# Performance work log

Hardware: AMD Instinct MI355X
Metric: run time of the kernel (lower is better)

Reference implementation:

```python
import jax, jax.numpy as jnp
import numpy as np

NEG_SLOPE = 0.2
N_NODES = 50000
N_EDGES = 800000
NUM_GRAPHS = 128
IN_F, HID_F, OUT_F = 64, 64, 64


def _gat_layer(x, src, dst, W, a_src, a_dst, b, n_nodes):
    # x: [N, Fin] -> out: [N, Fout]; single-head PyG GATConv with self-loops
    xp = x @ W                                   # [N, Fout]
    alpha_src = xp @ a_src                       # [N]
    alpha_dst = xp @ a_dst                       # [N]
    e = jax.nn.leaky_relu(alpha_src[src] + alpha_dst[dst], NEG_SLOPE)  # [E]
    # segment softmax over incoming edges of each dst node
    m = jax.ops.segment_max(e, dst, num_segments=n_nodes)
    ex = jnp.exp(e - m[dst])
    denom = jax.ops.segment_sum(ex, dst, num_segments=n_nodes)
    alpha = ex / denom[dst]                      # [E]
    out = jax.ops.segment_sum(alpha[:, None] * xp[src], dst, num_segments=n_nodes)
    return out + b


def setup_inputs() -> dict:
    key = jax.random.key(0)
    ks = jax.random.split(key, 12)
    x = jax.random.normal(ks[0], (N_NODES, IN_F), dtype=jnp.float32)
    edge_index = jax.random.randint(ks[1], (2, N_EDGES), 0, N_NODES, dtype=jnp.int64 if jax.config.jax_enable_x64 else jnp.int32)
    batch = jnp.sort(jax.random.randint(ks[2], (N_NODES,), 0, NUM_GRAPHS, dtype=edge_index.dtype))
    s = 0.1
    W1 = jax.random.normal(ks[3], (IN_F, HID_F), dtype=jnp.float32) * s
    att_src1 = jax.random.normal(ks[4], (HID_F,), dtype=jnp.float32) * s
    att_dst1 = jax.random.normal(ks[5], (HID_F,), dtype=jnp.float32) * s
    b1 = jax.random.normal(ks[6], (HID_F,), dtype=jnp.float32) * s
    W2 = jax.random.normal(ks[7], (HID_F, OUT_F), dtype=jnp.float32) * s
    att_src2 = jax.random.normal(ks[8], (OUT_F,), dtype=jnp.float32) * s
    att_dst2 = jax.random.normal(ks[9], (OUT_F,), dtype=jnp.float32) * s
    b2 = jax.random.normal(ks[10], (OUT_F,), dtype=jnp.float32) * s
    return {"x": x, "edge_index": edge_index, "batch": batch,
            "W1": W1, "att_src1": att_src1, "att_dst1": att_dst1, "b1": b1,
            "W2": W2, "att_src2": att_src2, "att_dst2": att_dst2, "b2": b2}


def reference(x, edge_index, batch, W1, att_src1, att_dst1, b1, W2, att_src2, att_dst2, b2):
    n = x.shape[0]
    # add self-loops (PyG GATConv default)
    loops = jnp.arange(n, dtype=edge_index.dtype)
    src = jnp.concatenate([edge_index[0], loops])
    dst = jnp.concatenate([edge_index[1], loops])
    h = _gat_layer(x, src, dst, W1, att_src1, att_dst1, b1, n)
    h = jax.nn.relu(h)  # dropout = identity at eval
    h = _gat_layer(h, src, dst, W2, att_src2, att_dst2, b2, n)
    h = jax.nn.relu(h)
    # scatter_mean over graphs
    sums = jax.ops.segment_sum(h, batch, num_segments=NUM_GRAPHS)
    counts = jax.ops.segment_sum(jnp.ones((n,), dtype=h.dtype), batch, num_segments=NUM_GRAPHS)
    return sums / jnp.maximum(counts, 1.0)[:, None]
```

## Files before the change

### kernel.cpp

```cpp
#include <hip/hip_runtime.h>
#include <hip/hip_fp16.h>

#define FEAT 64
#define BK   64
#define CAP  1536
#define MAXB 1024
#define SEPT 16
#define CHUNK (256 * SEPT)
#define LG   4

typedef _Float16 f16;
typedef __attribute__((ext_vector_type(8))) _Float16 f16x8;
typedef __attribute__((ext_vector_type(4))) float    f32x4;

struct GemmSm {
    union {
        struct { f16 Xs[64][72]; f16 Wt[64][72]; };
        float Cs[4][16][68];
    };
    float asl[64], adl[64];
};

__device__ __forceinline__ void gemm_tile(
    GemmSm& sm, int row0, const float* __restrict__ xin,
    const float* __restrict__ W, const float* __restrict__ avs,
    const float* __restrict__ avd, unsigned* __restrict__ xph,
    float* __restrict__ as_, float* __restrict__ ad_, int n)
{
    const int t = threadIdx.x;
    const int lane = t & 63;
    const int wave = t >> 6;

    if (t < 64) sm.asl[t] = avs[t];
    else if (t < 128) sm.adl[t - 64] = avd[t - 64];

    for (int i = t; i < 64 * 16; i += 256) {
        const int r = i >> 4, c4 = (i & 15) << 2;
        const int gr = row0 + r;
        float4 v = make_float4(0.f, 0.f, 0.f, 0.f);
        if (gr < n) v = *(const float4*)(xin + (size_t)gr * FEAT + c4);
        sm.Xs[r][c4 + 0] = (f16)v.x; sm.Xs[r][c4 + 1] = (f16)v.y;
        sm.Xs[r][c4 + 2] = (f16)v.z; sm.Xs[r][c4 + 3] = (f16)v.w;
    }
    for (int i = t; i < 64 * 16; i += 256) {
        const int k = i >> 4, c4 = (i & 15) << 2;
        const float4 v = *(const float4*)(W + k * FEAT + c4);
        sm.Wt[c4 + 0][k] = (f16)v.x; sm.Wt[c4 + 1][k] = (f16)v.y;
        sm.Wt[c4 + 2][k] = (f16)v.z; sm.Wt[c4 + 3][k] = (f16)v.w;
    }
    __syncthreads();

    const int mrow = (wave << 4) + (lane & 15);
    const int kg = lane >> 4;
    const f16x8 a0 = *(const f16x8*)(&sm.Xs[mrow][kg * 8]);
    const f16x8 a1 = *(const f16x8*)(&sm.Xs[mrow][32 + kg * 8]);

    f32x4 acc[4];
#pragma unroll
    for (int nt = 0; nt < 4; ++nt) {
        const int ncol = nt * 16 + (lane & 15);
        const f16x8 b0 = *(const f16x8*)(&sm.Wt[ncol][kg * 8]);
        const f16x8 b1 = *(const f16x8*)(&sm.Wt[ncol][32 + kg * 8]);
        f32x4 c = {0.f, 0.f, 0.f, 0.f};
        c = __builtin_amdgcn_mfma_f32_16x16x32_f16(a0, b0, c, 0, 0, 0);
        c = __builtin_amdgcn_mfma_f32_16x16x32_f16(a1, b1, c, 0, 0, 0);
        acc[nt] = c;
    }
    __syncthreads();

#pragma unroll
    for (int nt = 0; nt < 4; ++nt)
#pragma unroll
        for (int reg = 0; reg < 4; ++reg)
            sm.Cs[wave][(lane >> 4) * 4 + reg][nt * 16 + (lane & 15)] = acc[nt][reg];

    for (int i = lane; i < 16 * 32; i += 64) {
        const int r = i >> 5, fp = i & 31;
        const int node = row0 + (wave << 4) + r;
        if (node < n) {
            const __half2 pk = __floats2half2_rn(sm.Cs[wave][r][2 * fp],
                                                 sm.Cs[wave][r][2 * fp + 1]);
            xph[(size_t)node * 32 + fp] = *(const unsigned*)&pk;
        }
    }
    {
        const int r = lane >> 2, q = lane & 3;
        float s1 = 0.f, s2 = 0.f;
#pragma unroll
        for (int j = 0; j < 16; ++j) {
            const int c = q * 16 + j;
            const float v = sm.Cs[wave][r][c];
            s1 += v * sm.asl[c];
            s2 += v * sm.adl[c];
        }
        s1 += __shfl_xor(s1, 1); s1 += __shfl_xor(s1, 2);
        s2 += __shfl_xor(s2, 1); s2 += __shfl_xor(s2, 2);
        const int node = row0 + (wave << 4) + r;
        if (q == 0 && node < n) { as_[node] = s1; ad_[node] = s2; }
    }
}

__global__ __launch_bounds__(256) void scatter_gemm1_kernel(
    const int* __restrict__ src, const int* __restrict__ dst,
    int* __restrict__ bcur, unsigned* __restrict__ ebuf,
    const float* __restrict__ x, const float* __restrict__ W,
    const float* __restrict__ a_src, const float* __restrict__ a_dst,
    unsigned* __restrict__ xph, float* __restrict__ as_, float* __restrict__ ad_,
    int n, int E, int nbuck, int nchunks)
{
    __shared__ union {
        struct {
            unsigned staged[CHUNK];
            int hist[MAXB]; int lofs[MAXB]; int base[MAXB];
        } s;
        GemmSm g;
    } sm;

    const int t = threadIdx.x;
    const int lane = t & 63;
    const int wave = t >> 6;

    if (blockIdx.x < (unsigned)nchunks) {
        for (int i = t; i < nbuck; i += 256) sm.s.hist[i] = 0;
        __syncthreads();

        const int e0 = blockIdx.x * CHUNK;
        const int total = min(E - e0, CHUNK);

        unsigned code[SEPT]; int bk[SEPT], rk[SEPT];
#pragma unroll
        for (int k = 0; k < SEPT; ++k) {
            const int e = e0 + t + k * 256;
            bk[k] = -1;
            if (e < E) {
                const int s_ = src[e], d = dst[e];
                bk[k] = d >> 6;
                code[k] = ((unsigned)s_ << 6) | (unsigned)(d & 63);
                rk[k] = atomicAdd(&sm.s.hist[bk[k]], 1);
            }
        }
        __syncthreads();

        if (wave == 0) {
            int carry = 0;
            for (int b0 = 0; b0 < nbuck; b0 += 64) {
                const int idx = b0 + lane;
                int v = (idx < nbuck) ? sm.s.hist[idx] : 0;
                const int orig = v;
#pragma unroll
                for (int o = 1; o < 64; o <<= 1) {
                    const int u = __shfl_up(v, o);
                    if (lane >= o) v += u;
                }
                if (idx < nbuck) sm.s.lofs[idx] = v - orig + carry;
                carry += __shfl(v, 63);
            }
        }
        __syncthreads();
        for (int i = t; i < nbuck; i += 256) {
            const int hv = sm.s.hist[i];
            sm.s.base[i] = hv ? atomicAdd(&bcur[i], hv) : 0;
        }
        __syncthreads();

#pragma unroll
        for (int k = 0; k < SEPT; ++k) {
            if (bk[k] >= 0)
                sm.s.staged[sm.s.lofs[bk[k]] + rk[k]] =
                    ((unsigned)bk[k] << 22) | code[k];
        }
        __syncthreads();

        for (int i = t; i < total; i += 256) {
            const unsigned e = sm.s.staged[i];
            const int bkt = e >> 22;
            const int pos = sm.s.base[bkt] + (i - sm.s.lofs[bkt]);
            if (pos < CAP) ebuf[(size_t)bkt * CAP + pos] = e & 0x3FFFFFu;
        }
    } else {
        gemm_tile(sm.g, (blockIdx.x - nchunks) * 64, x, W, a_src, a_dst,
                  xph, as_, ad_, n);
    }
}

struct PC {
    int node, g, gc, st, en;
    float w0, w1, w2, w3, asg;
    uint4 x0, x1, x2, x3, xg;
};

__device__ __forceinline__ void fma8(float* a, const uint4 xv, const float wv)
{
    const __half2 p0 = *(const __half2*)&xv.x;
    const __half2 p1 = *(const __half2*)&xv.y;
    const __half2 p2 = *(const __half2*)&xv.z;
    const __half2 p3 = *(const __half2*)&xv.w;
    a[0] += wv * __low2float(p0);  a[1] += wv * __high2float(p0);
    a[2] += wv * __low2float(p1);  a[3] += wv * __high2float(p1);
    a[4] += wv * __low2float(p2);  a[5] += wv * __high2float(p2);
    a[6] += wv * __low2float(p3);  a[7] += wv * __high2float(p3);
}

__device__ __forceinline__ void pc_issue(PC& P, int pair, int np, int q, int fo,
    int g0, int n, const int* startsL, const unsigned* scode, const float* sw,
    const float* __restrict__ as_, const uint4* __restrict__ xph4)
{
    P.node = pair * 2 + np;
    P.g  = g0 + P.node;
    P.gc = (P.g < n) ? P.g : (n - 1);
    P.st = startsL[P.node];
    P.en = startsL[P.node + 1];
    const int i0 = P.st + q;
    unsigned c0 = 0, c1 = 0, c2 = 0, c3 = 0;
    P.w0 = 0.f; P.w1 = 0.f; P.w2 = 0.f; P.w3 = 0.f;
    if (i0      < P.en) { c0 = scode[i0];      P.w0 = sw[i0]; }
    if (i0 + 4  < P.en) { c1 = scode[i0 + 4];  P.w1 = sw[i0 + 4]; }
    if (i0 + 8  < P.en) { c2 = scode[i0 + 8];  P.w2 = sw[i0 + 8]; }
    if (i0 + 12 < P.en) { c3 = scode[i0 + 12]; P.w3 = sw[i0 + 12]; }
    P.x0 = xph4[(size_t)(c0 >> 6) * 8 + fo];
    P.x1 = xph4[(size_t)(c1 >> 6) * 8 + fo];
    P.x2 = xph4[(size_t)(c2 >> 6) * 8 + fo];
    P.x3 = xph4[(size_t)(c3 >> 6) * 8 + fo];
    P.xg = xph4[(size_t)P.gc * 8 + fo];
    P.asg = as_[P.gc];
}

__device__ __forceinline__ void pc_consume(const PC& P, int q, int fo,
    const unsigned* scode, const float* sw, const uint4* __restrict__ xph4,
    float* a, float& wsum)
{
    fma8(a, P.x0, P.w0); fma8(a, P.x1, P.w1);
    fma8(a, P.x2, P.w2); fma8(a, P.x3, P.w3);
    wsum += (P.w0 + P.w1) + (P.w2 + P.w3);

    int i = P.st + q + 16;
    for (; i + 12 < P.en; i += 16) {
        const unsigned c0 = scode[i];
        const unsigned c1 = scode[i + 4];
        const unsigned c2 = scode[i + 8];
        const unsigned c3 = scode[i + 12];
        const float w0 = sw[i], w1 = sw[i + 4], w2 = sw[i + 8], w3 = sw[i + 12];
        const uint4 x0 = xph4[(size_t)(c0 >> 6) * 8 + fo];
        const uint4 x1 = xph4[(size_t)(c1 >> 6) * 8 + fo];
        const uint4 x2 = xph4[(size_t)(c2 >> 6) * 8 + fo];
        const uint4 x3 = xph4[(size_t)(c3 >> 6) * 8 + fo];
        fma8(a, x0, w0); fma8(a, x1, w1); fma8(a, x2, w2); fma8(a, x3, w3);
        wsum += (w0 + w1) + (w2 + w3);
    }
    for (; i < P.en; i += 4) {
        const unsigned c0 = scode[i];
        const float w0 = sw[i];
        const uint4 xv = xph4[(size_t)(c0 >> 6) * 8 + fo];
        fma8(a, xv, w0);
        wsum += w0;
    }
}

__device__ __forceinline__ void pc_reduce(float* a, float& wsum)
{
#pragma unroll
    for (int j = 0; j < 8; ++j) {
        a[j] += __shfl_xor(a[j], 8);
        a[j] += __shfl_xor(a[j], 16);
    }
    wsum += __shfl_xor(wsum, 8);
    wsum += __shfl_xor(wsum, 16);
}

__device__ __forceinline__ void pc_epi_h(const PC& P, int q, int fo,
    const float* adb, float* a, float wsum, const float4 bA, const float4 bB,
    float* __restrict__ hout, int hstride, int n)
{
    pc_reduce(a, wsum);
    float tt = P.asg + adb[P.node];
    tt = (tt >= 0.f) ? tt : 0.2f * tt;
    const float wself = __expf(tt);
    const __half2 s0 = *(const __half2*)&P.xg.x;
    const __half2 s1 = *(const __half2*)&P.xg.y;
    const __half2 s2 = *(const __half2*)&P.xg.z;
    const __half2 s3 = *(const __half2*)&P.xg.w;
    const float dinv = 1.f / (wsum + wself);

    if (q == 0 && P.g < n) {
        float4 vA, vB;
        vA.x = fmaxf((a[0] + wself * __low2float(s0))  * dinv + bA.x, 0.f);
        vA.y = fmaxf((a[1] + wself * __high2float(s0)) * dinv + bA.y, 0.f);
        vA.z = fmaxf((a[2] + wself * __low2float(s1))  * dinv + bA.z, 0.f);
        vA.w = fmaxf((a[3] + wself * __high2float(s1)) * dinv + bA.w, 0.f);
        vB.x = fmaxf((a[4] + wself * __low2float(s2))  * dinv + bB.x, 0.f);
        vB.y = fmaxf((a[5] + wself * __high2float(s2)) * dinv + bB.y, 0.f);
        vB.z = fmaxf((a[6] + wself * __low2float(s3))  * dinv + bB.z, 0.f);
        vB.w = fmaxf((a[7] + wself * __high2float(s3)) * dinv + bB.w, 0.f);
        *(float4*)(hout + (size_t)P.node * hstride + 8 * fo)     = vA;
        *(float4*)(hout + (size_t)P.node * hstride + 8 * fo + 4) = vB;
    }
}

__device__ __forceinline__ void pc_epi_pool(const PC& P, int q, int fo,
    int wave, int np, const float* adb, float* a, float wsum,
    const float4 bA, const float4 bB, const int* batchL, int gbase,
    float (*gpartW)[2][LG][FEAT], float* __restrict__ osum, int n)
{
    pc_reduce(a, wsum);
    float tt = P.asg + adb[P.node];
    tt = (tt >= 0.f) ? tt : 0.2f * tt;
    const float wself = __expf(tt);
    const __half2 s0 = *(const __half2*)&P.xg.x;
    const __half2 s1 = *(const __half2*)&P.xg.y;
    const __half2 s2 = *(const __half2*)&P.xg.z;
    const __half2 s3 = *(const __half2*)&P.xg.w;
    const float dinv = 1.f / (wsum + wself);

    if (q == 0 && P.g < n) {
        float4 vA, vB;
        vA.x = fmaxf((a[0] + wself * __low2float(s0))  * dinv + bA.x, 0.f);
        vA.y = fmaxf((a[1] + wself * __high2float(s0)) * dinv + bA.y, 0.f);
        vA.z = fmaxf((a[2] + wself * __low2float(s1))  * dinv + bA.z, 0.f);
        vA.w = fmaxf((a[3] + wself * __high2float(s1)) * dinv + bA.w, 0.f);
        vB.x = fmaxf((a[4] + wself * __low2float(s2))  * dinv + bB.x, 0.f);
        vB.y = fmaxf((a[5] + wself * __high2float(s2)) * dinv + bB.y, 0.f);
        vB.z = fmaxf((a[6] + wself * __low2float(s3))  * dinv + bB.z, 0.f);
        vB.w = fmaxf((a[7] + wself * __high2float(s3)) * dinv + bB.w, 0.f);

        const int lg = batchL[P.node] - gbase;
        if (lg < LG) {
            float* p = &gpartW[wave][np][lg][8 * fo];
            float4 oA = *(float4*)p;
            float4 oB = *(float4*)(p + 4);
            oA.x += vA.x; oA.y += vA.y; oA.z += vA.z; oA.w += vA.w;
            oB.x += vB.x; oB.y += vB.y; oB.z += vB.z; oB.w += vB.w;
            *(float4*)p = oA;
            *(float4*)(p + 4) = oB;
        } else {
            float* o = osum + (size_t)batchL[P.node] * FEAT + 8 * fo;
            atomicAdd(o + 0, vA.x); atomicAdd(o + 1, vA.y);
            atomicAdd(o + 2, vA.z); atomicAdd(o + 3, vA.w);
            atomicAdd(o + 4, vB.x); atomicAdd(o + 5, vB.y);
            atomicAdd(o + 6, vB.z); atomicAdd(o + 7, vB.w);
        }
    }
}

__global__ __launch_bounds__(512) void sortagg1_gemm2_kernel(
    const int* __restrict__ bcur, unsigned* __restrict__ ebuf,
    int* __restrict__ startsG,
    const float* __restrict__ asA, const float* __restrict__ adA,
    const uint4* __restrict__ xphA, const float* __restrict__ b1,
    const float* __restrict__ W2, const float* __restrict__ asrc2,
    const float* __restrict__ adst2,
    unsigned* __restrict__ xphB, float* __restrict__ asB, float* __restrict__ adB,
    int n)
{
    __shared__ float htile[64][68];
    __shared__ union {
        struct { unsigned scode[CAP]; float sw[CAP]; int hist[BK]; int cur[BK]; } a;
        GemmSm g;
    } sm;
    __shared__ int starts[BK + 1];
    __shared__ float adb[BK];

    const int b = blockIdx.x;
    const int t = threadIdx.x;
    const int lane = t & 63, wave = t >> 6;
    const int g0 = b * BK;
    const int row0 = g0;

    if (t < BK) {
        sm.a.hist[t] = 0;
        adb[t] = (g0 + t < n) ? adA[g0 + t] : 0.f;
    }
    __syncthreads();

    int cnt = bcur[b];
    if (cnt > CAP) cnt = CAP;
    unsigned* eb = ebuf + (size_t)b * CAP;

    unsigned c[3];
#pragma unroll
    for (int k = 0; k < 3; ++k) {
        const int i = t + k * 512;
        if (i < cnt) { c[k] = eb[i]; atomicAdd(&sm.a.hist[c[k] & 63], 1); }
    }
    __syncthreads();
    if (wave == 0) {
        int v = sm.a.hist[lane];
#pragma unroll
        for (int o = 1; o < 64; o <<= 1) {
            const int u = __shfl_up(v, o);
            if (lane >= o) v += u;
        }
        starts[lane + 1] = v;
        sm.a.cur[lane] = v - sm.a.hist[lane];
        if (lane == 0) starts[0] = 0;
    }
    __syncthreads();
#pragma unroll
    for (int k = 0; k < 3; ++k) {
        const int i = t + k * 512;
        if (i < cnt) { const int p = atomicAdd(&sm.a.cur[c[k] & 63], 1); sm.a.scode[p] = c[k]; }
    }
    __syncthreads();

    unsigned cc[3]; float vv[3];
#pragma unroll
    for (int k = 0; k < 3; ++k) {
        const int i = t + k * 512;
        if (i < cnt) { cc[k] = sm.a.scode[i]; eb[i] = cc[k]; vv[k] = asA[cc[k] >> 6]; }
    }
    if (t <= BK) startsG[b * (BK + 1) + t] = starts[t];
#pragma unroll
    for (int k = 0; k < 3; ++k) {
        const int i = t + k * 512;
        if (i < cnt) {
            float tt = vv[k] + adb[cc[k] & 63];
            tt = (tt >= 0.f) ? tt : 0.2f * tt;
            sm.a.sw[i] = __expf(tt);
        }
    }
    __syncthreads();

    {
        const int np = lane >> 5;
        const int q  = (lane >> 3) & 3;
        const int fo = lane & 7;
        const float4 bA = *(const float4*)(b1 + 8 * fo);
        const float4 bB = *(const float4*)(b1 + 8 * fo + 4);
#pragma unroll
        for (int gsel = 0; gsel < 2; ++gsel) {
            PC A, B;
            pc_issue(A, wave + 8 * gsel,      np, q, fo, g0, n,
                     starts, sm.a.scode, sm.a.sw, asA, xphA);
            pc_issue(B, wave + 8 * gsel + 16, np, q, fo, g0, n,
                     starts, sm.a.scode, sm.a.sw, asA, xphA);
            float aA[8] = {0.f, 0.f, 0.f, 0.f, 0.f, 0.f, 0.f, 0.f};
            float wsA = 0.f;
            pc_consume(A, q, fo, sm.a.scode, sm.a.sw, xphA, aA, wsA);
            pc_epi_h(A, q, fo, adb, aA, wsA, bA, bB, &htile[0][0], 68, n);
            float aB[8] = {0.f, 0.f, 0.f, 0.f, 0.f, 0.f, 0.f, 0.f};
            float wsB = 0.f;
            pc_consume(B, q, fo, sm.a.scode, sm.a.sw, xphA, aB, wsB);
            pc_epi_h(B, q, fo, adb, aB, wsB, bA, bB, &htile[0][0], 68, n);
        }
    }
    __syncthreads();

    if (t < 64) sm.g.asl[t] = asrc2[t];
    else if (t < 128) sm.g.adl[t - 64] = adst2[t - 64];

    for (int i = t; i < 64 * 16; i += 512) {
        const int r = i >> 4, c4 = (i & 15) << 2;
        const float4 v = *(const float4*)(&htile[r][c4]);
        sm.g.Xs[r][c4 + 0] = (f16)v.x; sm.g.Xs[r][c4 + 1] = (f16)v.y;
        sm.g.Xs[r][c4 + 2] = (f16)v.z; sm.g.Xs[r][c4 + 3] = (f16)v.w;
    }
    for (int i = t; i < 64 * 16; i += 512) {
        const int k = i >> 4, c4 = (i & 15) << 2;
        const float4 v = *(const float4*)(W2 + k * FEAT + c4);
        sm.g.Wt[c4 + 0][k] = (f16)v.x; sm.g.Wt[c4 + 1][k] = (f16)v.y;
        sm.g.Wt[c4 + 2][k] = (f16)v.z; sm.g.Wt[c4 + 3][k] = (f16)v.w;
    }
    __syncthreads();

    f32x4 acc[4];
    if (wave < 4) {
        const int mrow = (wave << 4) + (lane & 15);
        const int kg = lane >> 4;
        const f16x8 a0 = *(const f16x8*)(&sm.g.Xs[mrow][kg * 8]);
        const f16x8 a1 = *(const f16x8*)(&sm.g.Xs[mrow][32 + kg * 8]);
#pragma unroll
        for (int nt = 0; nt < 4; ++nt) {
            const int ncol = nt * 16 + (lane & 15);
            const f16x8 b0 = *(const f16x8*)(&sm.g.Wt[ncol][kg * 8]);
            const f16x8 b1v = *(const f16x8*)(&sm.g.Wt[ncol][32 + kg * 8]);
            f32x4 cacc = {0.f, 0.f, 0.f, 0.f};
            cacc = __builtin_amdgcn_mfma_f32_16x16x32_f16(a0, b0, cacc, 0, 0, 0);
            cacc = __builtin_amdgcn_mfma_f32_16x16x32_f16(a1, b1v, cacc, 0, 0, 0);
            acc[nt] = cacc;
        }
    }
    __syncthreads();
    if (wave < 4) {
#pragma unroll
        for (int nt = 0; nt < 4; ++nt)
#pragma unroll
            for (int reg = 0; reg < 4; ++reg)
                sm.g.Cs[wave][(lane >> 4) * 4 + reg][nt * 16 + (lane & 15)] = acc[nt][reg];
    }
    __syncthreads();

    for (int i = t; i < 64 * 32; i += 512) {
        const int r = i >> 5, fp = i & 31;
        const int node = row0 + r;
        if (node < n) {
            const __half2 pk = __floats2half2_rn(sm.g.Cs[r >> 4][r & 15][2 * fp],
                                                 sm.g.Cs[r >> 4][r & 15][2 * fp + 1]);
            xphB[(size_t)node * 32 + fp] = *(const unsigned*)&pk;
        }
    }
    if (t < 256) {
        const int r = t >> 2, q = t & 3;
        float s1 = 0.f, s2 = 0.f;
#pragma unroll
        for (int j = 0; j < 16; ++j) {
            const int cidx = q * 16 + j;
            const float v = sm.g.Cs[r >> 4][r & 15][cidx];
            s1 += v * sm.g.asl[cidx];
            s2 += v * sm.g.adl[cidx];
        }
        s1 += __shfl_xor(s1, 1); s1 += __shfl_xor(s1, 2);
        s2 += __shfl_xor(s2, 1); s2 += __shfl_xor(s2, 2);
        const int node = row0 + r;
        if (q == 0 && node < n) { asB[node] = s1; adB[node] = s2; }
    }
}

__global__ __launch_bounds__(512) void agg2_pool_kernel(
    const unsigned* __restrict__ ebuf, const int* __restrict__ startsG,
    const float* __restrict__ as_, const float* __restrict__ ad_,
    const uint4* __restrict__ xph4, const float* __restrict__ bias,
    const int* __restrict__ batch, float* __restrict__ gpart,
    float* __restrict__ osum, int n)
{
    __shared__ unsigned scode[CAP];
    __shared__ float    sw[CAP];
    __shared__ int startsL[BK + 1];
    __shared__ float adb[BK];
    __shared__ int batchL[BK];
    __shared__ float gpartW[8][2][LG][FEAT];

    const int b = blockIdx.x;
    const int t = threadIdx.x;
    const int lane = t & 63, wave = t >> 6;
    const int g0 = b * BK;

    if (t < BK) {
        const int g = g0 + t;
        adb[t] = (g < n) ? ad_[g] : 0.f;
        batchL[t] = batch[(g < n) ? g : (n - 1)];
    }
    if (t <= BK) startsL[t] = startsG[b * (BK + 1) + t];
    for (int i = t; i < 8 * 2 * LG * FEAT; i += 512) ((float*)gpartW)[i] = 0.f;
    __syncthreads();

    const int cnt = startsL[BK];
    const unsigned* eb = ebuf + (size_t)b * CAP;

    unsigned cc[3]; float vv[3];
#pragma unroll
    for (int k = 0; k < 3; ++k) {
        const int i = t + k * 512;
        if (i < cnt) { cc[k] = eb[i]; vv[k] = as_[cc[k] >> 6]; }
    }
#pragma unroll
    for (int k = 0; k < 3; ++k) {
        const int i = t + k * 512;
        if (i < cnt) {
            float tt = vv[k] + adb[cc[k] & 63];
            tt = (tt >= 0.f) ? tt : 0.2f * tt;
            scode[i] = cc[k]; sw[i] = __expf(tt);
        }
    }
    __syncthreads();

    {
        const int np = lane >> 5;
        const int q  = (lane >> 3) & 3;
        const int fo = lane & 7;
        const int gbase = batchL[0];
        const float4 bA = *(const float4*)(bias + 8 * fo);
        const float4 bB = *(const float4*)(bias + 8 * fo + 4);
#pragma unroll
        for (int gsel = 0; gsel < 2; ++gsel) {
            PC A, B;
            pc_issue(A, wave + 8 * gsel,      np, q, fo, g0, n,
                     startsL, scode, sw, as_, xph4);
            pc_issue(B, wave + 8 * gsel + 16, np, q, fo, g0, n,
                     startsL, scode, sw, as_, xph4);
            float aA[8] = {0.f, 0.f, 0.f, 0.f, 0.f, 0.f, 0.f, 0.f};
            float wsA = 0.f;
            pc_consume(A, q, fo, scode, sw, xph4, aA, wsA);
            pc_epi_pool(A, q, fo, wave, np, adb, aA, wsA, bA, bB,
                        batchL, gbase, gpartW, osum, n);
            float aB[8] = {0.f, 0.f, 0.f, 0.f, 0.f, 0.f, 0.f, 0.f};
            float wsB = 0.f;
            pc_consume(B, q, fo, scode, sw, xph4, aB, wsB);
            pc_epi_pool(B, q, fo, wave, np, adb, aB, wsB, bA, bB,
                        batchL, gbase, gpartW, osum, n);
        }
    }
    __syncthreads();

    if (t < LG * FEAT) {
        const int lg = t >> 6, f = t & 63;
        float s = 0.f;
#pragma unroll
        for (int w = 0; w < 8; ++w)
            s += gpartW[w][0][lg][f] + gpartW[w][1][lg][f];
        gpart[((size_t)b * LG + lg) * FEAT + f] = s;
    }
}

__device__ __forceinline__ int lower_bound_i(const int* a, int n, int key)
{
    int lo = 0, hi = n;
    while (lo < hi) {
        const int mid = (lo + hi) >> 1;
        if (a[mid] < key) lo = mid + 1; else hi = mid;
    }
    return lo;
}

__global__ __launch_bounds__(64) void pool_reduce_kernel(
    const float* __restrict__ gpart, const float* __restrict__ osum,
    const int* __restrict__ batch, float* __restrict__ out, int n, int G)
{
    const int g = blockIdx.x;
    const int lane = threadIdx.x;

    const int lo = lower_bound_i(batch, n, g);
    const int hi = lower_bound_i(batch, n, g + 1);

    float s = osum[(size_t)g * FEAT + lane];
    if (lo < hi) {
        const int b0 = lo >> 6, b1 = (hi - 1) >> 6;
        for (int b = b0; b <= b1; ++b) {
            const int base = batch[b << 6];
            const int lg = g - base;
            if (lg >= 0 && lg < LG)
                s += gpart[((size_t)b * LG + lg) * FEAT + lane];
        }
    }
    out[(size_t)g * FEAT + lane] = s / fmaxf((float)(hi - lo), 1.f);
}

extern "C" void kernel_launch(void* const* d_in, const int* in_sizes, int n_in,
                              void* d_out, int out_size, void* d_ws, size_t ws_size,
                              hipStream_t stream)
{
    const float* x      = (const float*)d_in[0];
    const int*   ei     = (const int*)d_in[1];
    const int*   batch  = (const int*)d_in[2];
    const float* W1     = (const float*)d_in[3];
    const float* asrc1  = (const float*)d_in[4];
    const float* adst1  = (const float*)d_in[5];
    const float* b1     = (const float*)d_in[6];
    const float* W2     = (const float*)d_in[7];
    const float* asrc2  = (const float*)d_in[8];
    const float* adst2  = (const float*)d_in[9];
    const float* b2     = (const float*)d_in[10];

    const int N = in_sizes[2];
    const int E = in_sizes[1] / 2;
    const int G = out_size / FEAT;

    const int* src = ei;
    const int* dst = ei + E;

    const int nbuck   = (N + BK - 1) / BK;
    const int nchunks = (E + CHUNK - 1) / CHUNK;
    const int gemmBlocks = (N + 63) / 64;

    unsigned* xphA    = (unsigned*)d_ws;
    unsigned* xphB    = xphA + (size_t)N * 32;
    float*    asA     = (float*)(xphB + (size_t)N * 32);
    float*    adA     = asA + N;
    float*    asB     = adA + N;
    float*    adB     = asB + N;
    int*      bcur    = (int*)(adB + N);
    float*    osum    = (float*)(bcur + nbuck);
    unsigned* ebuf    = (unsigned*)(osum + (size_t)G * FEAT);
    int*      startsG = (int*)(ebuf + (size_t)nbuck * CAP);
    float*    gpart   = (float*)(startsG + nbuck * (BK + 1));

    hipMemsetAsync(bcur, 0,
                   (size_t)nbuck * sizeof(int) + (size_t)G * FEAT * sizeof(float),
                   stream);
    scatter_gemm1_kernel<<<nchunks + gemmBlocks, 256, 0, stream>>>(
        src, dst, bcur, ebuf, x, W1, asrc1, adst1, xphA, asA, adA,
        N, E, nbuck, nchunks);
    sortagg1_gemm2_kernel<<<nbuck, 512, 0, stream>>>(
        bcur, ebuf, startsG, asA, adA, (const uint4*)xphA, b1,
        W2, asrc2, adst2, xphB, asB, adB, N);
    agg2_pool_kernel<<<nbuck, 512, 0, stream>>>(
        ebuf, startsG, asB, adB, (const uint4*)xphB, b2,
        batch, gpart, osum, N);
    pool_reduce_kernel<<<G, 64, 0, stream>>>(gpart, osum, batch,
                                             (float*)d_out, N, G);
}
```

Baseline: 171.6 us.

## Remap aggregation to one node per wave with 8 edges in flight

The aggregation mapping changes from two nodes per wave (8 feature lanes × 4 edge lanes, uint4 loads) to one node per wave (16 feature lanes × 4 edge lanes, uint2 loads), with 8 gathers issued up front per lane. This gives more memory-level parallelism per node and drops the 16-wide unrolled loop. Layer-1 output is written straight into an fp16 shared tile that feeds the MFMA GEMM, removing the fp32 htile and its conversion pass. Pool partials are now added to osum with atomics inside agg2, so the final kernel only normalises, at the cost of extra global atomics and launch-bounds occupancy hints.

Result: slower. 179.5 us (+4.6%).

```diff
diff --git a/kernel.cpp b/kernel.cpp
--- a/kernel.cpp
+++ b/kernel.cpp
@@ -183,175 +183,143 @@
     }
 }
 
-struct PC {
+struct PC2 {
     int node, g, gc, st, en;
-    float w0, w1, w2, w3, asg;
-    uint4 x0, x1, x2, x3, xg;
+    float w[8], asg;
+    uint2 xs[8], xg;
 };
 
-__device__ __forceinline__ void fma8(float* a, const uint4 xv, const float wv)
+__device__ __forceinline__ void fma4(float* a, const uint2 xv, const float wv)
 {
     const __half2 p0 = *(const __half2*)&xv.x;
     const __half2 p1 = *(const __half2*)&xv.y;
-    const __half2 p2 = *(const __half2*)&xv.z;
-    const __half2 p3 = *(const __half2*)&xv.w;
-    a[0] += wv * __low2float(p0);  a[1] += wv * __high2float(p0);
-    a[2] += wv * __low2float(p1);  a[3] += wv * __high2float(p1);
-    a[4] += wv * __low2float(p2);  a[5] += wv * __high2float(p2);
-    a[6] += wv * __low2float(p3);  a[7] += wv * __high2float(p3);
-}
-
-__device__ __forceinline__ void pc_issue(PC& P, int pair, int np, int q, int fo,
+    a[0] += wv * __low2float(p0); a[1] += wv * __high2float(p0);
+    a[2] += wv * __low2float(p1); a[3] += wv * __high2float(p1);
+}
+
+__device__ __forceinline__ void pc2_issue(PC2& P, int node, int q, int fo,
     int g0, int n, const int* startsL, const unsigned* scode, const float* sw,
-    const float* __restrict__ as_, const uint4* __restrict__ xph4)
-{
-    P.node = pair * 2 + np;
-    P.g  = g0 + P.node;
+    const float* __restrict__ as_, const uint2* __restrict__ xph2)
+{
+    P.node = node;
+    P.g  = g0 + node;
     P.gc = (P.g < n) ? P.g : (n - 1);
-    P.st = startsL[P.node];
-    P.en = startsL[P.node + 1];
+    P.st = startsL[node];
+    P.en = startsL[node + 1];
     const int i0 = P.st + q;
-    unsigned c0 = 0, c1 = 0, c2 = 0, c3 = 0;
-    P.w0 = 0.f; P.w1 = 0.f; P.w2 = 0.f; P.w3 = 0.f;
-    if (i0      < P.en) { c0 = scode[i0];      P.w0 = sw[i0]; }
-    if (i0 + 4  < P.en) { c1 = scode[i0 + 4];  P.w1 = sw[i0 + 4]; }
-    if (i0 + 8  < P.en) { c2 = scode[i0 + 8];  P.w2 = sw[i0 + 8]; }
-    if (i0 + 12 < P.en) { c3 = scode[i0 + 12]; P.w3 = sw[i0 + 12]; }
-    P.x0 = xph4[(size_t)(c0 >> 6) * 8 + fo];
-    P.x1 = xph4[(size_t)(c1 >> 6) * 8 + fo];
-    P.x2 = xph4[(size_t)(c2 >> 6) * 8 + fo];
-    P.x3 = xph4[(size_t)(c3 >> 6) * 8 + fo];
-    P.xg = xph4[(size_t)P.gc * 8 + fo];
+    unsigned c[8];
+#pragma unroll
+    for (int j = 0; j < 8; ++j) {
+        const int i = i0 + 4 * j;
+        c[j] = 0u; P.w[j] = 0.f;
+        if (i < P.en) { c[j] = scode[i]; P.w[j] = sw[i]; }
+    }
+#pragma unroll
+    for (int j = 0; j < 8; ++j)
+        P.xs[j] = xph2[(size_t)(c[j] >> 6) * 16 + fo];
+    P.xg = xph2[(size_t)P.gc * 16 + fo];
     P.asg = as_[P.gc];
 }
 
-__device__ __forceinline__ void pc_consume(const PC& P, int q, int fo,
-    const unsigned* scode, const float* sw, const uint4* __restrict__ xph4,
+__device__ __forceinline__ void pc2_consume(const PC2& P, int q, int fo,
+    const unsigned* scode, const float* sw, const uint2* __restrict__ xph2,
     float* a, float& wsum)
 {
-    fma8(a, P.x0, P.w0); fma8(a, P.x1, P.w1);
-    fma8(a, P.x2, P.w2); fma8(a, P.x3, P.w3);
-    wsum += (P.w0 + P.w1) + (P.w2 + P.w3);
-
-    int i = P.st + q + 16;
-    for (; i + 12 < P.en; i += 16) {
-        const unsigned c0 = scode[i];
-        const unsigned c1 = scode[i + 4];
-        const unsigned c2 = scode[i + 8];
-        const unsigned c3 = scode[i + 12];
-        const float w0 = sw[i], w1 = sw[i + 4], w2 = sw[i + 8], w3 = sw[i + 12];
-        const uint4 x0 = xph4[(size_t)(c0 >> 6) * 8 + fo];
-        const uint4 x1 = xph4[(size_t)(c1 >> 6) * 8 + fo];
-        const uint4 x2 = xph4[(size_t)(c2 >> 6) * 8 + fo];
-        const uint4 x3 = xph4[(size_t)(c3 >> 6) * 8 + fo];
-        fma8(a, x0, w0); fma8(a, x1, w1); fma8(a, x2, w2); fma8(a, x3, w3);
-        wsum += (w0 + w1) + (w2 + w3);
-    }
-    for (; i < P.en; i += 4) {
+#pragma unroll
+    for (int j = 0; j < 8; ++j) { fma4(a, P.xs[j], P.w[j]); wsum += P.w[j]; }
+    for (int i = P.st + q + 32; i < P.en; i += 4) {
         const unsigned c0 = scode[i];
         const float w0 = sw[i];
-        const uint4 xv = xph4[(size_t)(c0 >> 6) * 8 + fo];
-        fma8(a, xv, w0);
-        wsum += w0;
-    }
-}
-
-__device__ __forceinline__ void pc_reduce(float* a, float& wsum)
-{
-#pragma unroll
-    for (int j = 0; j < 8; ++j) {
-        a[j] += __shfl_xor(a[j], 8);
+        const uint2 xv = xph2[(size_t)(c0 >> 6) * 16 + fo];
+        fma4(a, xv, w0); wsum += w0;
+    }
+}
+
+__device__ __forceinline__ void pc2_reduce(float* a, float& wsum)
+{
+#pragma unroll
+    for (int j = 0; j < 4; ++j) {
         a[j] += __shfl_xor(a[j], 16);
-    }
-    wsum += __shfl_xor(wsum, 8);
+        a[j] += __shfl_xor(a[j], 32);
+    }
     wsum += __shfl_xor(wsum, 16);
-}
-
-__device__ __forceinline__ void pc_epi_h(const PC& P, int q, int fo,
-    const float* adb, float* a, float wsum, const float4 bA, const float4 bB,
-    float* __restrict__ hout, int hstride, int n)
-{
-    pc_reduce(a, wsum);
+    wsum += __shfl_xor(wsum, 32);
+}
+
+__device__ __forceinline__ void pc2_epi_h(const PC2& P, int q, int fo,
+    const float* adb, float* a, float wsum, const float4 bb,
+    f16* __restrict__ ht, int n)
+{
+    pc2_reduce(a, wsum);
     float tt = P.asg + adb[P.node];
     tt = (tt >= 0.f) ? tt : 0.2f * tt;
     const float wself = __expf(tt);
     const __half2 s0 = *(const __half2*)&P.xg.x;
     const __half2 s1 = *(const __half2*)&P.xg.y;
-    const __half2 s2 = *(const __half2*)&P.xg.z;
-    const __half2 s3 = *(const __half2*)&P.xg.w;
     const float dinv = 1.f / (wsum + wself);
 
-    if (q == 0 && P.g < n) {
-        float4 vA, vB;
-        vA.x = fmaxf((a[0] + wself * __low2float(s0))  * dinv + bA.x, 0.f);
-        vA.y = fmaxf((a[1] + wself * __high2float(s0)) * dinv + bA.y, 0.f);
-        vA.z = fmaxf((a[2] + wself * __low2float(s1))  * dinv + bA.z, 0.f);
-        vA.w = fmaxf((a[3] + wself * __high2float(s1)) * dinv + bA.w, 0.f);
-        vB.x = fmaxf((a[4] + wself * __low2float(s2))  * dinv + bB.x, 0.f);
-        vB.y = fmaxf((a[5] + wself * __high2float(s2)) * dinv + bB.y, 0.f);
-        vB.z = fmaxf((a[6] + wself * __low2float(s3))  * dinv + bB.z, 0.f);
-        vB.w = fmaxf((a[7] + wself * __high2float(s3)) * dinv + bB.w, 0.f);
-        *(float4*)(hout + (size_t)P.node * hstride + 8 * fo)     = vA;
-        *(float4*)(hout + (size_t)P.node * hstride + 8 * fo + 4) = vB;
-    }
-}
-
-__device__ __forceinline__ void pc_epi_pool(const PC& P, int q, int fo,
-    int wave, int np, const float* adb, float* a, float wsum,
-    const float4 bA, const float4 bB, const int* batchL, int gbase,
-    float (*gpartW)[2][LG][FEAT], float* __restrict__ osum, int n)
-{
-    pc_reduce(a, wsum);
+    if (q == 0) {
+        float4 v = make_float4(0.f, 0.f, 0.f, 0.f);
+        if (P.g < n) {
+            v.x = fmaxf((a[0] + wself * __low2float(s0))  * dinv + bb.x, 0.f);
+            v.y = fmaxf((a[1] + wself * __high2float(s0)) * dinv + bb.y, 0.f);
+            v.z = fmaxf((a[2] + wself * __low2float(s1))  * dinv + bb.z, 0.f);
+            v.w = fmaxf((a[3] + wself * __high2float(s1)) * dinv + bb.w, 0.f);
+        }
+        const __half2 h01 = __floats2half2_rn(v.x, v.y);
+        const __half2 h23 = __floats2half2_rn(v.z, v.w);
+        uint2 pk;
+        pk.x = *(const unsigned*)&h01;
+        pk.y = *(const unsigned*)&h23;
+        *(uint2*)(ht + (size_t)P.node * 72 + fo * 4) = pk;
+    }
+}
+
+__device__ __forceinline__ void pc2_epi_pool(const PC2& P, int q, int fo,
+    int wave, const float* adb, float* a, float wsum, const float4 bb,
+    const int* batchL, int gbase, float (*gpartW)[LG][FEAT],
+    float* __restrict__ osum, int n)
+{
+    pc2_reduce(a, wsum);
     float tt = P.asg + adb[P.node];
     tt = (tt >= 0.f) ? tt : 0.2f * tt;
     const float wself = __expf(tt);
     const __half2 s0 = *(const __half2*)&P.xg.x;
     const __half2 s1 = *(const __half2*)&P.xg.y;
-    const __half2 s2 = *(const __half2*)&P.xg.z;
-    const __half2 s3 = *(const __half2*)&P.xg.w;
     const float dinv = 1.f / (wsum + wself);
 
     if (q == 0 && P.g < n) {
-        float4 vA, vB;
-        vA.x = fmaxf((a[0] + wself * __low2float(s0))  * dinv + bA.x, 0.f);
-        vA.y = fmaxf((a[1] + wself * __high2float(s0)) * dinv + bA.y, 0.f);
-        vA.z = fmaxf((a[2] + wself * __low2float(s1))  * dinv + bA.z, 0.f);
-        vA.w = fmaxf((a[3] + wself * __high2float(s1)) * dinv + bA.w, 0.f);
-        vB.x = fmaxf((a[4] + wself * __low2float(s2))  * dinv + bB.x, 0.f);
-        vB.y = fmaxf((a[5] + wself * __high2float(s2)) * dinv + bB.y, 0.f);
-        vB.z = fmaxf((a[6] + wself * __low2float(s3))  * dinv + bB.z, 0.f);
-        vB.w = fmaxf((a[7] + wself * __high2float(s3)) * dinv + bB.w, 0.f);
+        float4 v;
+        v.x = fmaxf((a[0] + wself * __low2float(s0))  * dinv + bb.x, 0.f);
+        v.y = fmaxf((a[1] + wself * __high2float(s0)) * dinv + bb.y, 0.f);
+        v.z = fmaxf((a[2] + wself * __low2float(s1))  * dinv + bb.z, 0.f);
+        v.w = fmaxf((a[3] + wself * __high2float(s1)) * dinv + bb.w, 0.f);
 
         const int lg = batchL[P.node] - gbase;
         if (lg < LG) {
-            float* p = &gpartW[wave][np][lg][8 * fo];
-            float4 oA = *(float4*)p;
-            float4 oB = *(float4*)(p + 4);
-            oA.x += vA.x; oA.y += vA.y; oA.z += vA.z; oA.w += vA.w;
-            oB.x += vB.x; oB.y += vB.y; oB.z += vB.z; oB.w += vB.w;
-            *(float4*)p = oA;
-            *(float4*)(p + 4) = oB;
+            float* p = &gpartW[wave][lg][4 * fo];
+            float4 o = *(float4*)p;
+            o.x += v.x; o.y += v.y; o.z += v.z; o.w += v.w;
+            *(float4*)p = o;
         } else {
-            float* o = osum + (size_t)batchL[P.node] * FEAT + 8 * fo;
-            atomicAdd(o + 0, vA.x); atomicAdd(o + 1, vA.y);
-            atomicAdd(o + 2, vA.z); atomicAdd(o + 3, vA.w);
-            atomicAdd(o + 4, vB.x); atomicAdd(o + 5, vB.y);
-            atomicAdd(o + 6, vB.z); atomicAdd(o + 7, vB.w);
-        }
-    }
-}
-
-__global__ __launch_bounds__(512) void sortagg1_gemm2_kernel(
+            float* o = osum + (size_t)batchL[P.node] * FEAT + 4 * fo;
+            atomicAdd(o + 0, v.x); atomicAdd(o + 1, v.y);
+            atomicAdd(o + 2, v.z); atomicAdd(o + 3, v.w);
+        }
+    }
+}
+
+__global__ __launch_bounds__(512, 4) void sortagg1_gemm2_kernel(
     const int* __restrict__ bcur, unsigned* __restrict__ ebuf,
     int* __restrict__ startsG,
     const float* __restrict__ asA, const float* __restrict__ adA,
-    const uint4* __restrict__ xphA, const float* __restrict__ b1,
+    const uint2* __restrict__ xphA, const float* __restrict__ b1,
     const float* __restrict__ W2, const float* __restrict__ asrc2,
     const float* __restrict__ adst2,
     unsigned* __restrict__ xphB, float* __restrict__ asB, float* __restrict__ adB,
     int n)
 {
-    __shared__ float htile[64][68];
+    __shared__ f16 ht16[64][72];
     __shared__ union {
         struct { unsigned scode[CAP]; float sw[CAP]; int hist[BK]; int cur[BK]; } a;
         GemmSm g;
@@ -420,26 +388,22 @@
     __syncthreads();
 
     {
-        const int np = lane >> 5;
-        const int q  = (lane >> 3) & 3;
-        const int fo = lane & 7;
-        const float4 bA = *(const float4*)(b1 + 8 * fo);
-        const float4 bB = *(const float4*)(b1 + 8 * fo + 4);
-#pragma unroll
-        for (int gsel = 0; gsel < 2; ++gsel) {
-            PC A, B;
-            pc_issue(A, wave + 8 * gsel,      np, q, fo, g0, n,
-                     starts, sm.a.scode, sm.a.sw, asA, xphA);
-            pc_issue(B, wave + 8 * gsel + 16, np, q, fo, g0, n,
-                     starts, sm.a.scode, sm.a.sw, asA, xphA);
-            float aA[8] = {0.f, 0.f, 0.f, 0.f, 0.f, 0.f, 0.f, 0.f};
-            float wsA = 0.f;
-            pc_consume(A, q, fo, sm.a.scode, sm.a.sw, xphA, aA, wsA);
-            pc_epi_h(A, q, fo, adb, aA, wsA, bA, bB, &htile[0][0], 68, n);
-            float aB[8] = {0.f, 0.f, 0.f, 0.f, 0.f, 0.f, 0.f, 0.f};
-            float wsB = 0.f;
-            pc_consume(B, q, fo, sm.a.scode, sm.a.sw, xphA, aB, wsB);
-            pc_epi_h(B, q, fo, adb, aB, wsB, bA, bB, &htile[0][0], 68, n);
+        const int q  = lane >> 4;
+        const int fo = lane & 15;
+        const float4 bb = *(const float4*)(b1 + 4 * fo);
+#pragma unroll
+        for (int gsel = 0; gsel < 4; ++gsel) {
+            PC2 A, B;
+            pc2_issue(A, wave + 16 * gsel,     q, fo, g0, n,
+                      starts, sm.a.scode, sm.a.sw, asA, xphA);
+            pc2_issue(B, wave + 16 * gsel + 8, q, fo, g0, n,
+                      starts, sm.a.scode, sm.a.sw, asA, xphA);
+            float aA[4] = {0.f, 0.f, 0.f, 0.f}; float wsA = 0.f;
+            pc2_consume(A, q, fo, sm.a.scode, sm.a.sw, xphA, aA, wsA);
+            pc2_epi_h(A, q, fo, adb, aA, wsA, bb, &ht16[0][0], n);
+            float aB[4] = {0.f, 0.f, 0.f, 0.f}; float wsB = 0.f;
+            pc2_consume(B, q, fo, sm.a.scode, sm.a.sw, xphA, aB, wsB);
+            pc2_epi_h(B, q, fo, adb, aB, wsB, bb, &ht16[0][0], n);
         }
     }
     __syncthreads();
@@ -447,12 +411,6 @@
     if (t < 64) sm.g.asl[t] = asrc2[t];
     else if (t < 128) sm.g.adl[t - 64] = adst2[t - 64];
 
-    for (int i = t; i < 64 * 16; i += 512) {
-        const int r = i >> 4, c4 = (i & 15) << 2;
-        const float4 v = *(const float4*)(&htile[r][c4]);
-        sm.g.Xs[r][c4 + 0] = (f16)v.x; sm.g.Xs[r][c4 + 1] = (f16)v.y;
-        sm.g.Xs[r][c4 + 2] = (f16)v.z; sm.g.Xs[r][c4 + 3] = (f16)v.w;
-    }
     for (int i = t; i < 64 * 16; i += 512) {
         const int k = i >> 4, c4 = (i & 15) << 2;
         const float4 v = *(const float4*)(W2 + k * FEAT + c4);
@@ -465,8 +423,8 @@
     if (wave < 4) {
         const int mrow = (wave << 4) + (lane & 15);
         const int kg = lane >> 4;
-        const f16x8 a0 = *(const f16x8*)(&sm.g.Xs[mrow][kg * 8]);
-        const f16x8 a1 = *(const f16x8*)(&sm.g.Xs[mrow][32 + kg * 8]);
+        const f16x8 a0 = *(const f16x8*)(&ht16[mrow][kg * 8]);
+        const f16x8 a1 = *(const f16x8*)(&ht16[mrow][32 + kg * 8]);
 #pragma unroll
         for (int nt = 0; nt < 4; ++nt) {
             const int ncol = nt * 16 + (lane & 15);
@@ -514,19 +472,18 @@
     }
 }
 
-__global__ __launch_bounds__(512) void agg2_pool_kernel(
+__global__ __launch_bounds__(512, 4) void agg2_pool_kernel(
     const unsigned* __restrict__ ebuf, const int* __restrict__ startsG,
     const float* __restrict__ as_, const float* __restrict__ ad_,
-    const uint4* __restrict__ xph4, const float* __restrict__ bias,
-    const int* __restrict__ batch, float* __restrict__ gpart,
-    float* __restrict__ osum, int n)
+    const uint2* __restrict__ xph2, const float* __restrict__ bias,
+    const int* __restrict__ batch, float* __restrict__ osum, int n, int G)
 {
     __shared__ unsigned scode[CAP];
     __shared__ float    sw[CAP];
     __shared__ int startsL[BK + 1];
     __shared__ float adb[BK];
     __shared__ int batchL[BK];
-    __shared__ float gpartW[8][2][LG][FEAT];
+    __shared__ float gpartW[8][LG][FEAT];
 
     const int b = blockIdx.x;
     const int t = threadIdx.x;
@@ -539,7 +496,7 @@
         batchL[t] = batch[(g < n) ? g : (n - 1)];
     }
     if (t <= BK) startsL[t] = startsG[b * (BK + 1) + t];
-    for (int i = t; i < 8 * 2 * LG * FEAT; i += 512) ((float*)gpartW)[i] = 0.f;
+    for (int i = t; i < 8 * LG * FEAT; i += 512) ((float*)gpartW)[i] = 0.f;
     __syncthreads();
 
     const int cnt = startsL[BK];
@@ -563,29 +520,25 @@
     __syncthreads();
 
     {
-        const int np = lane >> 5;
-        const int q  = (lane >> 3) & 3;
-        const int fo = lane & 7;
+        const int q  = lane >> 4;
+        const int fo = lane & 15;
         const int gbase = batchL[0];
-        const float4 bA = *(const float4*)(bias + 8 * fo);
-        const float4 bB = *(const float4*)(bias + 8 * fo + 4);
-#pragma unroll
-        for (int gsel = 0; gsel < 2; ++gsel) {
-            PC A, B;
-            pc_issue(A, wave + 8 * gsel,      np, q, fo, g0, n,
-                     startsL, scode, sw, as_, xph4);
-            pc_issue(B, wave + 8 * gsel + 16, np, q, fo, g0, n,
-                     startsL, scode, sw, as_, xph4);
-            float aA[8] = {0.f, 0.f, 0.f, 0.f, 0.f, 0.f, 0.f, 0.f};
-            float wsA = 0.f;
-            pc_consume(A, q, fo, scode, sw, xph4, aA, wsA);
-            pc_epi_pool(A, q, fo, wave, np, adb, aA, wsA, bA, bB,
-                        batchL, gbase, gpartW, osum, n);
-            float aB[8] = {0.f, 0.f, 0.f, 0.f, 0.f, 0.f, 0.f, 0.f};
-            float wsB = 0.f;
-            pc_consume(B, q, fo, scode, sw, xph4, aB, wsB);
-            pc_epi_pool(B, q, fo, wave, np, adb, aB, wsB, bA, bB,
-                        batchL, gbase, gpartW, osum, n);
+        const float4 bb = *(const float4*)(bias + 4 * fo);
+#pragma unroll
+        for (int gsel = 0; gsel < 4; ++gsel) {
+            PC2 A, B;
+            pc2_issue(A, wave + 16 * gsel,     q, fo, g0, n,
+                      startsL, scode, sw, as_, xph2);
+            pc2_issue(B, wave + 16 * gsel + 8, q, fo, g0, n,
+                      startsL, scode, sw, as_, xph2);
+            float aA[4] = {0.f, 0.f, 0.f, 0.f}; float wsA = 0.f;
+            pc2_consume(A, q, fo, scode, sw, xph2, aA, wsA);
+            pc2_epi_pool(A, q, fo, wave, adb, aA, wsA, bb,
+                         batchL, gbase, gpartW, osum, n);
+            float aB[4] = {0.f, 0.f, 0.f, 0.f}; float wsB = 0.f;
+            pc2_consume(B, q, fo, scode, sw, xph2, aB, wsB);
+            pc2_epi_pool(B, q, fo, wave, adb, aB, wsB, bb,
+                         batchL, gbase, gpartW, osum, n);
         }
     }
     __syncthreads();
@@ -595,8 +548,10 @@
         float s = 0.f;
 #pragma unroll
         for (int w = 0; w < 8; ++w)
-            s += gpartW[w][0][lg][f] + gpartW[w][1][lg][f];
-        gpart[((size_t)b * LG + lg) * FEAT + f] = s;
+            s += gpartW[w][lg][f];
+        const int gg = batchL[0] + lg;
+        if (s != 0.f && gg < G)
+            atomicAdd(&osum[(size_t)gg * FEAT + f], s);
     }
 }
 
@@ -610,27 +565,16 @@
     return lo;
 }
 
-__global__ __launch_bounds__(64) void pool_reduce_kernel(
-    const float* __restrict__ gpart, const float* __restrict__ osum,
-    const int* __restrict__ batch, float* __restrict__ out, int n, int G)
+__global__ __launch_bounds__(64) void pool_norm_kernel(
+    const float* __restrict__ osum, const int* __restrict__ batch,
+    float* __restrict__ out, int n, int G)
 {
     const int g = blockIdx.x;
     const int lane = threadIdx.x;
-
     const int lo = lower_bound_i(batch, n, g);
     const int hi = lower_bound_i(batch, n, g + 1);
-
-    float s = osum[(size_t)g * FEAT + lane];
-    if (lo < hi) {
-        const int b0 = lo >> 6, b1 = (hi - 1) >> 6;
-        for (int b = b0; b <= b1; ++b) {
-            const int base = batch[b << 6];
-            const int lg = g - base;
-            if (lg >= 0 && lg < LG)
-                s += gpart[((size_t)b * LG + lg) * FEAT + lane];
-        }
-    }
-    out[(size_t)g * FEAT + lane] = s / fmaxf((float)(hi - lo), 1.f);
+    out[(size_t)g * FEAT + lane] =
+        osum[(size_t)g * FEAT + lane] / fmaxf((float)(hi - lo), 1.f);
 }
 
 extern "C" void kernel_launch(void* const* d_in, const int* in_sizes, int n_in,
@@ -670,7 +614,6 @@
     float*    osum    = (float*)(bcur + nbuck);
     unsigned* ebuf    = (unsigned*)(osum + (size_t)G * FEAT);
     int*      startsG = (int*)(ebuf + (size_t)nbuck * CAP);
-    float*    gpart   = (float*)(startsG + nbuck * (BK + 1));
 
     hipMemsetAsync(bcur, 0,
                    (size_t)nbuck * sizeof(int) + (size_t)G * FEAT * sizeof(float),
@@ -679,11 +622,10 @@
         src, dst, bcur, ebuf, x, W1, asrc1, adst1, xphA, asA, adA,
         N, E, nbuck, nchunks);
     sortagg1_gemm2_kernel<<<nbuck, 512, 0, stream>>>(
-        bcur, ebuf, startsG, asA, adA, (const uint4*)xphA, b1,
+        bcur, ebuf, startsG, asA, adA, (const uint2*)xphA, b1,
         W2, asrc2, adst2, xphB, asB, adB, N);
     agg2_pool_kernel<<<nbuck, 512, 0, stream>>>(
-        ebuf, startsG, asB, adB, (const uint4*)xphB, b2,
-        batch, gpart, osum, N);
-    pool_reduce_kernel<<<G, 64, 0, stream>>>(gpart, osum, batch,
-                                             (float*)d_out, N, G);
-}
+        ebuf, startsG, asB, adB, (const uint2*)xphB, b2,
+        batch, osum, N, G);
+    pool_norm_kernel<<<G, 64, 0, stream>>>(osum, batch, (float*)d_out, N, G);
+}
```
